# Performance work log

Measured on AMD Instinct MI355X. Metric: run time of the kernel, lower is better.

## Reference

```python
import jax, jax.numpy as jnp
import numpy as np

K = 7          # kernel_size (window)
PAD = (K - 1) // 2  # SAME padding for stride 1


def setup_inputs() -> dict:
    key = jax.random.key(0)
    ks = jax.random.split(key, 7)
    B, H, W, C, F = 8, 128, 128, 256, 256
    rs = F // 2  # rel_size
    return {
        "x": jax.random.normal(ks[0], (B, H, W, C), jnp.float32),
        "Wq": jax.random.normal(ks[1], (C, F), jnp.float32) * 0.05,
        "Wk": jax.random.normal(ks[2], (C, F), jnp.float32) * 0.05,
        "Wv": jax.random.normal(ks[3], (C, F), jnp.float32) * 0.05,
        "rel_x": jax.random.normal(ks[4], (rs, K), jnp.float32) * 0.05,
        "rel_y": jax.random.normal(ks[5], (F - rs, K), jnp.float32) * 0.05,
        "bias": jax.random.normal(ks[6], (1, 1, 1, F), jnp.float32) * (1.0 / np.sqrt(F).astype(np.float32)),
    }


def reference(x, Wq, Wk, Wv, rel_x, rel_y, bias):
    B, H, W, C = x.shape
    rs = rel_x.shape[0]
    # 1x1 conv projections (single group)
    q = jnp.einsum('bhwc,cf->bhwf', x, Wq)
    k = jnp.einsum('bhwc,cf->bhwf', x, Wk)
    v = jnp.einsum('bhwc,cf->bhwf', x, Wv)
    kp = jnp.pad(k, ((0, 0), (PAD, PAD), (PAD, PAD), (0, 0)))
    vp = jnp.pad(v, ((0, 0), (PAD, PAD), (PAD, PAD), (0, 0)))
    # window scores: sum_c q * shifted(k) -> [b,h,w,kh,kw]; avoids im2col blowup
    scores = jnp.stack([
        jnp.stack([jnp.einsum('bhwf,bhwf->bhw', q, kp[:, i:i + H, j:j + W, :])
                   for j in range(K)], axis=-1)
        for i in range(K)], axis=-2)
    # relative position terms: x-half broadcasts along rows (kh), y-half along cols (kw)
    qx = jnp.einsum('bhwx,xk->bhwk', q[..., :rs], rel_x)
    qy = jnp.einsum('bhwy,yk->bhwk', q[..., rs:], rel_y)
    scores = scores + qx[:, :, :, None, :] + qy[:, :, :, :, None]
    attn = jax.nn.softmax(scores.reshape(B, H, W, K * K), axis=-1).reshape(B, H, W, K, K)
    # attention-weighted sum over the window for each channel
    out = sum(attn[:, :, :, i, j][..., None] * vp[:, i:i + H, j:j + W, :]
              for i in range(K) for j in range(K))
    return out + bias
```

## Files before the change

### kernel.cpp

```cpp
#include <hip/hip_runtime.h>
#include <hip/hip_fp16.h>
#include <stdint.h>

typedef _Float16 half8 __attribute__((ext_vector_type(8)));
typedef _Float16 half2v __attribute__((ext_vector_type(2)));
typedef __attribute__((ext_vector_type(4))) float f32x4;

__device__ __forceinline__ unsigned short f2h(float f) {
  __half h = __float2half(f);
  unsigned short u; __builtin_memcpy(&u, &h, 2); return u;
}
__device__ __forceinline__ unsigned pk2h(float a, float b) {
  auto v = __builtin_amdgcn_cvt_pkrtz(a, b);
  unsigned u; __builtin_memcpy(&u, &v, 4); return u;
}
__device__ __forceinline__ half2v h2cast(unsigned u) {
  half2v v; __builtin_memcpy(&v, &u, 4); return v;
}

#if __has_builtin(__builtin_amdgcn_fdot2)
__device__ __forceinline__ float dot2(half2v a, half2v b, float c) {
  return __builtin_amdgcn_fdot2(a, b, c, false);
}
#else
__device__ __forceinline__ float dot2(half2v a, half2v b, float c) {
  return c + (float)a[0] * (float)b[0] + (float)a[1] * (float)b[1];
}
#endif

__device__ __forceinline__ void gl_lds16(const void* g, void* l) {
  __builtin_amdgcn_global_load_lds(
      (const __attribute__((address_space(1))) void*)g,
      (__attribute__((address_space(3))) void*)l, 16, 0, 0);
}

__global__ __launch_bounds__(256) void xcvt(const float* __restrict__ x,
                                            unsigned short* __restrict__ xh) {
  const size_t i = ((size_t)blockIdx.x * 256 + threadIdx.x) * 8;
  float4 a = *(const float4*)&x[i];
  float4 b = *(const float4*)&x[i + 4];
  uint4 o;
  o.x = pk2h(a.x, a.y); o.y = pk2h(a.z, a.w);
  o.z = pk2h(b.x, b.y); o.w = pk2h(b.z, b.w);
  *(uint4*)&xh[i] = o;
}

__global__ __launch_bounds__(256) void wconv(const float* __restrict__ Wq,
                                             const float* __restrict__ Wk,
                                             const float* __restrict__ Wv,
                                             unsigned short* __restrict__ Wb) {
  const int e = blockIdx.x;
  const int w = e >> 8;
  const int n = e & 255;
  const float* W = (w == 0) ? Wq : ((w == 1) ? Wk : Wv);
  const int k = threadIdx.x;
  Wb[(size_t)e * 256 + k] = f2h(W[(size_t)k * 256 + n]);
}

__global__ __launch_bounds__(256) void qkv_gemm(const unsigned short* __restrict__ xh,
                                                const unsigned short* __restrict__ Wb,
                                                unsigned short* __restrict__ qkv) {
  __shared__ unsigned char ldsb[32768];

  const int tid = threadIdx.x;
  const int l = tid & 63, l15 = l & 15, l4 = l >> 4;
  const int wv = tid >> 6, wr = wv >> 1, wc = wv & 1;

  const int pid = blockIdx.x;
  const int cid = (pid & 7) * 768 + (pid >> 3);
  const int by = cid / 6;
  const int bx = cid - by * 6;
  const size_t row0 = (size_t)by * 128;
  const int n0 = bx * 128;

  const int rbase0 = wv * 32, rbase1 = wv * 32 + 16;
  const int rA0 = rbase0 + (l >> 2), rA1 = rbase1 + (l >> 2);
  const int q0 = (l & 3) ^ ((rA0 >> 1) & 3), q1 = (l & 3) ^ ((rA1 >> 1) & 3);
  const unsigned short* gA0 = xh + (row0 + rA0) * 256 + q0 * 8;
  const unsigned short* gA1 = xh + (row0 + rA1) * 256 + q1 * 8;
  const unsigned short* gB0 = Wb + (size_t)(n0 + rA0) * 256 + q0 * 8;
  const unsigned short* gB1 = Wb + (size_t)(n0 + rA1) * 256 + q1 * 8;

  f32x4 acc[4][4] = {};

  auto stage = [&](int s, int d) {
    gl_lds16(gA0 + s * 32, &ldsb[d * 8192 + rbase0 * 64]);
    gl_lds16(gA1 + s * 32, &ldsb[d * 8192 + rbase1 * 64]);
    gl_lds16(gB0 + s * 32, &ldsb[16384 + d * 8192 + rbase0 * 64]);
    gl_lds16(gB1 + s * 32, &ldsb[16384 + d * 8192 + rbase1 * 64]);
  };

  stage(0, 0);
  __syncthreads();

  for (int s = 0; s < 8; ++s) {
    const int d = s & 1;
    if (s < 7) stage(s + 1, d ^ 1);
    half8 af[4], bf[4];
#pragma unroll
    for (int m = 0; m < 4; ++m) {
      const int r = wr * 64 + m * 16 + l15;
      af[m] = *(const half8*)&ldsb[d * 8192 + r * 64 + ((l4 ^ ((r >> 1) & 3)) * 16)];
    }
#pragma unroll
    for (int n = 0; n < 4; ++n) {
      const int r = wc * 64 + n * 16 + l15;
      bf[n] = *(const half8*)&ldsb[16384 + d * 8192 + r * 64 + ((l4 ^ ((r >> 1) & 3)) * 16)];
    }
#pragma unroll
    for (int n = 0; n < 4; ++n)
#pragma unroll
      for (int m = 0; m < 4; ++m)
        acc[m][n] = __builtin_amdgcn_mfma_f32_16x16x32_f16(af[m], bf[n], acc[m][n], 0, 0, 0);
    __syncthreads();
  }

#pragma unroll
  for (int m = 0; m < 4; ++m)
#pragma unroll
    for (int n = 0; n < 4; ++n) {
      const int ng = n0 + wc * 64 + n * 16 + l15;
      unsigned short* op = qkv + (size_t)(ng >> 8) * 33554432 + (ng & 255);
#pragma unroll
      for (int r = 0; r < 4; ++r) {
        const size_t grow = row0 + wr * 64 + m * 16 + l4 * 4 + r;
        op[grow * 256] = f2h(acc[m][n][r]);
      }
    }
}

__global__ __launch_bounds__(256) void qrel(const unsigned short* __restrict__ q,
                                            const float* __restrict__ relx,
                                            const float* __restrict__ rely,
                                            unsigned short* __restrict__ qr) {
  __shared__ unsigned wpk[896];
  for (int i = threadIdx.x; i < 896; i += 256) {
    const int hf = (i >= 448) ? 1 : 0;
    const int r = i - hf * 448;
    const int c2 = r / 7, j = r - c2 * 7;
    const float* R = hf ? rely : relx;
    wpk[i] = pk2h(R[(2 * c2) * 7 + j], R[(2 * c2 + 1) * 7 + j]);
  }
  __syncthreads();
  const size_t pix = (size_t)blockIdx.x * 256 + threadIdx.x;
  const uint4* qp = (const uint4*)(q + pix * 256);
  float ax[7] = {0, 0, 0, 0, 0, 0, 0}, ay[7] = {0, 0, 0, 0, 0, 0, 0};
#pragma unroll
  for (int g = 0; g < 32; ++g) {
    const uint4 u = qp[g];
    const int c2b = (g & 15) * 4;
    if (g < 16) {
#pragma unroll
      for (int j = 0; j < 7; ++j) {
        float s = ax[j];
        s = dot2(h2cast(u.x), h2cast(wpk[(c2b + 0) * 7 + j]), s);
        s = dot2(h2cast(u.y), h2cast(wpk[(c2b + 1) * 7 + j]), s);
        s = dot2(h2cast(u.z), h2cast(wpk[(c2b + 2) * 7 + j]), s);
        s = dot2(h2cast(u.w), h2cast(wpk[(c2b + 3) * 7 + j]), s);
        ax[j] = s;
      }
    } else {
#pragma unroll
      for (int j = 0; j < 7; ++j) {
        float s = ay[j];
        s = dot2(h2cast(u.x), h2cast(wpk[448 + (c2b + 0) * 7 + j]), s);
        s = dot2(h2cast(u.y), h2cast(wpk[448 + (c2b + 1) * 7 + j]), s);
        s = dot2(h2cast(u.z), h2cast(wpk[448 + (c2b + 2) * 7 + j]), s);
        s = dot2(h2cast(u.w), h2cast(wpk[448 + (c2b + 3) * 7 + j]), s);
        ay[j] = s;
      }
    }
  }
  uint4 o0, o1;
  o0.x = pk2h(ax[0], ax[1]); o0.y = pk2h(ax[2], ax[3]);
  o0.z = pk2h(ax[4], ax[5]); o0.w = pk2h(ax[6], ay[0]);
  o1.x = pk2h(ay[1], ay[2]); o1.y = pk2h(ay[3], ay[4]);
  o1.z = pk2h(ay[5], ay[6]); o1.w = 0;
  uint4* dst = (uint4*)(qr + pix * 512);
  dst[0] = o0; dst[1] = o1;
}

__global__ __launch_bounds__(256) void attn(const unsigned short* __restrict__ qkv,
                                            const float* __restrict__ bias,
                                            const unsigned short* __restrict__ qrelb,
                                            float* __restrict__ out) {
  __shared__ unsigned short kv[532 * 40];

  const int tid = threadIdx.x;
  const int col = tid & 31, row = tid >> 5;

  const int pid = blockIdx.x;
  const int cid = (pid & 7) * 64 + (pid >> 3);
  const int ht = cid & 15, wt = (cid >> 4) & 3, b = cid >> 6;

  const int h = ht * 8 + row, w = wt * 32 + col;
  const size_t pix = (size_t)((b * 128 + h) * 128 + w);
  const int pbase = (row * 38 + col) * 40;

  const unsigned short* qb = qkv;
  const unsigned short* kb = qkv + 33554432;
  const unsigned short* vb = qkv + 67108864;

  auto stage = [&](const unsigned short* base, int f0) {
    for (int p = tid; p < 532; p += 256) {
      const int pr = p / 38, pc = p - pr * 38;
      const int gh = ht * 8 + pr - 3, gw = wt * 32 + pc - 3;
      uint4 v0 = make_uint4(0, 0, 0, 0), v1 = v0, v2 = v0, v3 = v0;
      if ((unsigned)gh < 128u && (unsigned)gw < 128u) {
        const uint4* src = (const uint4*)(base + ((size_t)((b * 128 + gh) * 128 + gw) * 256 + f0));
        v0 = src[0]; v1 = src[1]; v2 = src[2]; v3 = src[3];
      }
      uint4* d = (uint4*)&kv[p * 40];
      d[0] = v0; d[1] = v1; d[2] = v2; d[3] = v3;
    }
  };

  float qx[7], qy[7];
  {
    const uint4* rp = (const uint4*)(qrelb + pix * 512);
    uint4 r0 = rp[0], r1 = rp[1];
    half2v a0 = h2cast(r0.x), a1 = h2cast(r0.y), a2 = h2cast(r0.z), a3 = h2cast(r0.w);
    half2v b0 = h2cast(r1.x), b1 = h2cast(r1.y), b2 = h2cast(r1.z);
    qx[0] = a0[0]; qx[1] = a0[1]; qx[2] = a1[0]; qx[3] = a1[1];
    qx[4] = a2[0]; qx[5] = a2[1]; qx[6] = a3[0];
    qy[0] = a3[1]; qy[1] = b0[0]; qy[2] = b0[1]; qy[3] = b1[0];
    qy[4] = b1[1]; qy[5] = b2[0]; qy[6] = b2[1];
  }

  float sc[49];
#pragma unroll
  for (int t = 0; t < 49; ++t) sc[t] = 0.0f;

  for (int c = 0; c < 8; ++c) {
    const int f0 = c * 32;
    __syncthreads();
    stage(kb, f0);
    __syncthreads();
    const uint4* qsrc = (const uint4*)(qb + pix * 256 + f0);
    uint4 u0 = qsrc[0], u1 = qsrc[1], u2 = qsrc[2], u3 = qsrc[3];
    half2v qh[16];
    qh[0] = h2cast(u0.x); qh[1] = h2cast(u0.y); qh[2] = h2cast(u0.z); qh[3] = h2cast(u0.w);
    qh[4] = h2cast(u1.x); qh[5] = h2cast(u1.y); qh[6] = h2cast(u1.z); qh[7] = h2cast(u1.w);
    qh[8] = h2cast(u2.x); qh[9] = h2cast(u2.y); qh[10] = h2cast(u2.z); qh[11] = h2cast(u2.w);
    qh[12] = h2cast(u3.x); qh[13] = h2cast(u3.y); qh[14] = h2cast(u3.z); qh[15] = h2cast(u3.w);
#pragma unroll
    for (int i = 0; i < 7; ++i)
#pragma unroll
      for (int j = 0; j < 7; ++j) {
        const uint4* kp = (const uint4*)&kv[pbase + (i * 38 + j) * 40];
        uint4 k0 = kp[0], k1 = kp[1], k2 = kp[2], k3 = kp[3];
        float s = sc[i * 7 + j];
        s = dot2(h2cast(k0.x), qh[0], s);  s = dot2(h2cast(k0.y), qh[1], s);
        s = dot2(h2cast(k0.z), qh[2], s);  s = dot2(h2cast(k0.w), qh[3], s);
        s = dot2(h2cast(k1.x), qh[4], s);  s = dot2(h2cast(k1.y), qh[5], s);
        s = dot2(h2cast(k1.z), qh[6], s);  s = dot2(h2cast(k1.w), qh[7], s);
        s = dot2(h2cast(k2.x), qh[8], s);  s = dot2(h2cast(k2.y), qh[9], s);
        s = dot2(h2cast(k2.z), qh[10], s); s = dot2(h2cast(k2.w), qh[11], s);
        s = dot2(h2cast(k3.x), qh[12], s); s = dot2(h2cast(k3.y), qh[13], s);
        s = dot2(h2cast(k3.z), qh[14], s); s = dot2(h2cast(k3.w), qh[15], s);
        sc[i * 7 + j] = s;
      }
  }

#pragma unroll
  for (int i = 0; i < 7; ++i)
#pragma unroll
    for (int j = 0; j < 7; ++j) sc[i * 7 + j] += qx[j] + qy[i];
  float mx = sc[0];
#pragma unroll
  for (int t = 1; t < 49; ++t) mx = fmaxf(mx, sc[t]);
  float sum = 0.0f;
#pragma unroll
  for (int t = 0; t < 49; ++t) {
    float e = __expf(sc[t] - mx);
    sc[t] = e;
    sum += e;
  }
  const float invs = 1.0f / sum;
  unsigned pw[49];
#pragma unroll
  for (int t = 0; t < 49; ++t) {
    const unsigned short ph = f2h(sc[t] * invs);
    pw[t] = (unsigned)ph | ((unsigned)ph << 16);
  }

  for (int c = 0; c < 8; ++c) {
    const int f0 = c * 32;
    __syncthreads();
    stage(vb, f0);
    __syncthreads();
    half2v acc[16];
#pragma unroll
    for (int a = 0; a < 16; ++a) acc[a] = half2v{(_Float16)0, (_Float16)0};
#pragma unroll
    for (int i = 0; i < 7; ++i)
#pragma unroll
      for (int j = 0; j < 7; ++j) {
        const uint4* vp = (const uint4*)&kv[pbase + (i * 38 + j) * 40];
        uint4 v0 = vp[0], v1 = vp[1], v2 = vp[2], v3 = vp[3];
        const half2v p2 = h2cast(pw[i * 7 + j]);
        acc[0] += p2 * h2cast(v0.x);  acc[1] += p2 * h2cast(v0.y);
        acc[2] += p2 * h2cast(v0.z);  acc[3] += p2 * h2cast(v0.w);
        acc[4] += p2 * h2cast(v1.x);  acc[5] += p2 * h2cast(v1.y);
        acc[6] += p2 * h2cast(v1.z);  acc[7] += p2 * h2cast(v1.w);
        acc[8] += p2 * h2cast(v2.x);  acc[9] += p2 * h2cast(v2.y);
        acc[10] += p2 * h2cast(v2.z); acc[11] += p2 * h2cast(v2.w);
        acc[12] += p2 * h2cast(v3.x); acc[13] += p2 * h2cast(v3.y);
        acc[14] += p2 * h2cast(v3.z); acc[15] += p2 * h2cast(v3.w);
      }
#pragma unroll
    for (int fq = 0; fq < 8; ++fq) {
      float4 bv = *(const float4*)&bias[f0 + fq * 4];
      float4 o;
      o.x = (float)acc[fq * 2 + 0][0] + bv.x;
      o.y = (float)acc[fq * 2 + 0][1] + bv.y;
      o.z = (float)acc[fq * 2 + 1][0] + bv.z;
      o.w = (float)acc[fq * 2 + 1][1] + bv.w;
      *(float4*)&out[pix * 256 + f0 + fq * 4] = o;
    }
  }
}

extern "C" void kernel_launch(void* const* d_in, const int* in_sizes, int n_in,
                              void* d_out, int out_size, void* d_ws, size_t ws_size,
                              hipStream_t stream) {
  const float* x = (const float*)d_in[0];
  const float* Wq = (const float*)d_in[1];
  const float* Wk = (const float*)d_in[2];
  const float* Wv = (const float*)d_in[3];
  const float* relx = (const float*)d_in[4];
  const float* rely = (const float*)d_in[5];
  const float* bias = (const float*)d_in[6];
  float* out = (float*)d_out;

  unsigned short* xh = (unsigned short*)d_out;
  unsigned short* qrl = (unsigned short*)d_out;
  unsigned short* Wb = (unsigned short*)d_ws;
  unsigned short* qkv = (unsigned short*)((char*)d_ws + 393216);

  xcvt<<<dim3(16384), dim3(256), 0, stream>>>(x, xh);
  wconv<<<dim3(768), dim3(256), 0, stream>>>(Wq, Wk, Wv, Wb);
  qkv_gemm<<<dim3(6144), dim3(256), 0, stream>>>(xh, Wb, qkv);
  qrel<<<dim3(512), dim3(256), 0, stream>>>(qkv, relx, rely, qrl);
  attn<<<dim3(512), dim3(256), 0, stream>>>(qkv, bias, qrl, out);
}
```

Measured before the change: 283.4 us.

## Double-buffer K/V tiles with direct global-to-LDS loads and wave priority

Replaces the synchronous stage-then-compute loop in the attention kernel with a double-buffered pipeline. The next K or V channel chunk is fetched straight into LDS with global-to-LDS loads while the current chunk is computed, and the first V chunk is prefetched during the last K chunk. The LDS tile is re-laid out into four planar 8-half groups, halo zeros are written once, and the compute sections are wrapped in s_setprio. This aims to hide global load latency and remove a barrier per chunk, but it increases LDS use, which may lower occupancy.

```diff
diff --git a/kernel.cpp b/kernel.cpp
--- a/kernel.cpp
+++ b/kernel.cpp
@@ -184,7 +184,7 @@
                                             const float* __restrict__ bias,
                                             const unsigned short* __restrict__ qrelb,
                                             float* __restrict__ out) {
-  __shared__ unsigned short kv[532 * 40];
+  __shared__ unsigned short kv[2][4][4256];
 
   const int tid = threadIdx.x;
   const int col = tid & 31, row = tid >> 5;
@@ -195,25 +195,54 @@
 
   const int h = ht * 8 + row, w = wt * 32 + col;
   const size_t pix = (size_t)((b * 128 + h) * 128 + w);
-  const int pbase = (row * 38 + col) * 40;
+  const int pbase = row * 38 + col;
 
   const unsigned short* qb = qkv;
   const unsigned short* kb = qkv + 33554432;
   const unsigned short* vb = qkv + 67108864;
 
-  auto stage = [&](const unsigned short* base, int f0) {
+  const int pr0 = tid / 38, pc0 = tid - pr0 * 38;
+  const int gh0 = ht * 8 + pr0 - 3, gw0 = wt * 32 + pc0 - 3;
+  const bool ok0 = ((unsigned)gh0 < 128u) && ((unsigned)gw0 < 128u);
+  const long long go0 = ((long long)((b * 128 + gh0) * 128 + gw0)) * 256;
+
+  const int p1 = tid + 256;
+  const int pr1 = p1 / 38, pc1 = p1 - pr1 * 38;
+  const int gh1 = ht * 8 + pr1 - 3, gw1 = wt * 32 + pc1 - 3;
+  const bool ok1 = ((unsigned)gh1 < 128u) && ((unsigned)gw1 < 128u);
+  const long long go1 = ((long long)((b * 128 + gh1) * 128 + gw1)) * 256;
+
+  const int p2 = tid + 512;
+  const int pr2 = p2 / 38, pc2 = p2 - pr2 * 38;
+  const int gh2 = ht * 8 + pr2 - 3, gw2 = wt * 32 + pc2 - 3;
+  const bool ok2 = (p2 < 532) && ((unsigned)gh2 < 128u) && ((unsigned)gw2 < 128u);
+  const long long go2 = ((long long)((b * 128 + gh2) * 128 + gw2)) * 256;
+
+  const int wb8 = (tid >> 6) * 512;
+
+  auto stage = [&](const unsigned short* base, int c, int d) {
+#pragma unroll
+    for (int g = 0; g < 4; ++g) {
+      if (ok0) gl_lds16(base + go0 + c * 32 + g * 8, &kv[d][g][wb8]);
+      if (ok1) gl_lds16(base + go1 + c * 32 + g * 8, &kv[d][g][2048 + wb8]);
+      if (ok2) gl_lds16(base + go2 + c * 32 + g * 8, &kv[d][g][4096]);
+    }
+  };
+
+  {
+    const uint4 z = make_uint4(0u, 0u, 0u, 0u);
     for (int p = tid; p < 532; p += 256) {
       const int pr = p / 38, pc = p - pr * 38;
       const int gh = ht * 8 + pr - 3, gw = wt * 32 + pc - 3;
-      uint4 v0 = make_uint4(0, 0, 0, 0), v1 = v0, v2 = v0, v3 = v0;
-      if ((unsigned)gh < 128u && (unsigned)gw < 128u) {
-        const uint4* src = (const uint4*)(base + ((size_t)((b * 128 + gh) * 128 + gw) * 256 + f0));
-        v0 = src[0]; v1 = src[1]; v2 = src[2]; v3 = src[3];
-      }
-      uint4* d = (uint4*)&kv[p * 40];
-      d[0] = v0; d[1] = v1; d[2] = v2; d[3] = v3;
-    }
-  };
+      if (!((unsigned)gh < 128u && (unsigned)gw < 128u)) {
+#pragma unroll
+        for (int d = 0; d < 2; ++d)
+#pragma unroll
+          for (int g = 0; g < 4; ++g)
+            *(uint4*)&kv[d][g][p * 8] = z;
+      }
+    }
+  }
 
   float qx[7], qy[7];
   {
@@ -227,39 +256,46 @@
     qy[4] = b1[1]; qy[5] = b2[0]; qy[6] = b2[1];
   }
 
+  stage(kb, 0, 0);
+  __syncthreads();
+
   float sc[49];
 #pragma unroll
   for (int t = 0; t < 49; ++t) sc[t] = 0.0f;
 
-  for (int c = 0; c < 8; ++c) {
-    const int f0 = c * 32;
-    __syncthreads();
-    stage(kb, f0);
-    __syncthreads();
-    const uint4* qsrc = (const uint4*)(qb + pix * 256 + f0);
+  for (int s = 0; s < 8; ++s) {
+    const int d = s & 1;
+    stage(s < 7 ? kb : vb, s < 7 ? s + 1 : 0, d ^ 1);
+    const uint4* qsrc = (const uint4*)(qb + pix * 256 + s * 32);
     uint4 u0 = qsrc[0], u1 = qsrc[1], u2 = qsrc[2], u3 = qsrc[3];
     half2v qh[16];
     qh[0] = h2cast(u0.x); qh[1] = h2cast(u0.y); qh[2] = h2cast(u0.z); qh[3] = h2cast(u0.w);
     qh[4] = h2cast(u1.x); qh[5] = h2cast(u1.y); qh[6] = h2cast(u1.z); qh[7] = h2cast(u1.w);
     qh[8] = h2cast(u2.x); qh[9] = h2cast(u2.y); qh[10] = h2cast(u2.z); qh[11] = h2cast(u2.w);
     qh[12] = h2cast(u3.x); qh[13] = h2cast(u3.y); qh[14] = h2cast(u3.z); qh[15] = h2cast(u3.w);
+    __builtin_amdgcn_s_setprio(1);
 #pragma unroll
     for (int i = 0; i < 7; ++i)
 #pragma unroll
       for (int j = 0; j < 7; ++j) {
-        const uint4* kp = (const uint4*)&kv[pbase + (i * 38 + j) * 40];
-        uint4 k0 = kp[0], k1 = kp[1], k2 = kp[2], k3 = kp[3];
-        float s = sc[i * 7 + j];
-        s = dot2(h2cast(k0.x), qh[0], s);  s = dot2(h2cast(k0.y), qh[1], s);
-        s = dot2(h2cast(k0.z), qh[2], s);  s = dot2(h2cast(k0.w), qh[3], s);
-        s = dot2(h2cast(k1.x), qh[4], s);  s = dot2(h2cast(k1.y), qh[5], s);
-        s = dot2(h2cast(k1.z), qh[6], s);  s = dot2(h2cast(k1.w), qh[7], s);
-        s = dot2(h2cast(k2.x), qh[8], s);  s = dot2(h2cast(k2.y), qh[9], s);
-        s = dot2(h2cast(k2.z), qh[10], s); s = dot2(h2cast(k2.w), qh[11], s);
-        s = dot2(h2cast(k3.x), qh[12], s); s = dot2(h2cast(k3.y), qh[13], s);
-        s = dot2(h2cast(k3.z), qh[14], s); s = dot2(h2cast(k3.w), qh[15], s);
-        sc[i * 7 + j] = s;
-      }
+        const int q8 = (pbase + i * 38 + j) * 8;
+        uint4 k0 = *(const uint4*)&kv[d][0][q8];
+        uint4 k1 = *(const uint4*)&kv[d][1][q8];
+        uint4 k2 = *(const uint4*)&kv[d][2][q8];
+        uint4 k3 = *(const uint4*)&kv[d][3][q8];
+        float s2 = sc[i * 7 + j];
+        s2 = dot2(h2cast(k0.x), qh[0], s2);  s2 = dot2(h2cast(k0.y), qh[1], s2);
+        s2 = dot2(h2cast(k0.z), qh[2], s2);  s2 = dot2(h2cast(k0.w), qh[3], s2);
+        s2 = dot2(h2cast(k1.x), qh[4], s2);  s2 = dot2(h2cast(k1.y), qh[5], s2);
+        s2 = dot2(h2cast(k1.z), qh[6], s2);  s2 = dot2(h2cast(k1.w), qh[7], s2);
+        s2 = dot2(h2cast(k2.x), qh[8], s2);  s2 = dot2(h2cast(k2.y), qh[9], s2);
+        s2 = dot2(h2cast(k2.z), qh[10], s2); s2 = dot2(h2cast(k2.w), qh[11], s2);
+        s2 = dot2(h2cast(k3.x), qh[12], s2); s2 = dot2(h2cast(k3.y), qh[13], s2);
+        s2 = dot2(h2cast(k3.z), qh[14], s2); s2 = dot2(h2cast(k3.w), qh[15], s2);
+        sc[i * 7 + j] = s2;
+      }
+    __builtin_amdgcn_s_setprio(0);
+    __syncthreads();
   }
 
 #pragma unroll
@@ -284,30 +320,34 @@
     pw[t] = (unsigned)ph | ((unsigned)ph << 16);
   }
 
-  for (int c = 0; c < 8; ++c) {
-    const int f0 = c * 32;
-    __syncthreads();
-    stage(vb, f0);
-    __syncthreads();
+  for (int s = 0; s < 8; ++s) {
+    const int d = s & 1;
+    const int f0 = s * 32;
+    if (s < 7) stage(vb, s + 1, d ^ 1);
     half2v acc[16];
 #pragma unroll
     for (int a = 0; a < 16; ++a) acc[a] = half2v{(_Float16)0, (_Float16)0};
+    __builtin_amdgcn_s_setprio(1);
 #pragma unroll
     for (int i = 0; i < 7; ++i)
 #pragma unroll
       for (int j = 0; j < 7; ++j) {
-        const uint4* vp = (const uint4*)&kv[pbase + (i * 38 + j) * 40];
-        uint4 v0 = vp[0], v1 = vp[1], v2 = vp[2], v3 = vp[3];
-        const half2v p2 = h2cast(pw[i * 7 + j]);
-        acc[0] += p2 * h2cast(v0.x);  acc[1] += p2 * h2cast(v0.y);
-        acc[2] += p2 * h2cast(v0.z);  acc[3] += p2 * h2cast(v0.w);
-        acc[4] += p2 * h2cast(v1.x);  acc[5] += p2 * h2cast(v1.y);
-        acc[6] += p2 * h2cast(v1.z);  acc[7] += p2 * h2cast(v1.w);
-        acc[8] += p2 * h2cast(v2.x);  acc[9] += p2 * h2cast(v2.y);
-        acc[10] += p2 * h2cast(v2.z); acc[11] += p2 * h2cast(v2.w);
-        acc[12] += p2 * h2cast(v3.x); acc[13] += p2 * h2cast(v3.y);
-        acc[14] += p2 * h2cast(v3.z); acc[15] += p2 * h2cast(v3.w);
-      }
+        const int q8 = (pbase + i * 38 + j) * 8;
+        uint4 v0 = *(const uint4*)&kv[d][0][q8];
+        uint4 v1 = *(const uint4*)&kv[d][1][q8];
+        uint4 v2 = *(const uint4*)&kv[d][2][q8];
+        uint4 v3 = *(const uint4*)&kv[d][3][q8];
+        const half2v p2h = h2cast(pw[i * 7 + j]);
+        acc[0] += p2h * h2cast(v0.x);  acc[1] += p2h * h2cast(v0.y);
+        acc[2] += p2h * h2cast(v0.z);  acc[3] += p2h * h2cast(v0.w);
+        acc[4] += p2h * h2cast(v1.x);  acc[5] += p2h * h2cast(v1.y);
+        acc[6] += p2h * h2cast(v1.z);  acc[7] += p2h * h2cast(v1.w);
+        acc[8] += p2h * h2cast(v2.x);  acc[9] += p2h * h2cast(v2.y);
+        acc[10] += p2h * h2cast(v2.z); acc[11] += p2h * h2cast(v2.w);
+        acc[12] += p2h * h2cast(v3.x); acc[13] += p2h * h2cast(v3.y);
+        acc[14] += p2h * h2cast(v3.z); acc[15] += p2h * h2cast(v3.w);
+      }
+    __builtin_amdgcn_s_setprio(0);
 #pragma unroll
     for (int fq = 0; fq < 8; ++fq) {
       float4 bv = *(const float4*)&bias[f0 + fq * 4];
@@ -318,6 +358,7 @@
       o.w = (float)acc[fq * 2 + 1][1] + bv.w;
       *(float4*)&out[pix * 256 + f0 + fq * 4] = o;
     }
+    if (s < 7) __syncthreads();
   }
 }
 
```

Result: no change. 281.2 us (-0.8%).
